# Kernel optimization log

Hardware: AMD Instinct MI355X
Metric: run time of the kernel (lower is better)

The kernel has to match this reference:

```python
import jax, jax.numpy as jnp
import numpy as np

TAU = 0.1  # args.aggregator_tau


def _l2_normalize(x, eps=1e-12):
    # F.normalize(x) : dim=1, p=2, eps clamp on the norm
    n = jnp.linalg.norm(x, axis=1, keepdims=True)
    return x / jnp.maximum(n, eps)


def setup_inputs() -> dict:
    key = jax.random.key(0)
    ks = jax.random.split(key, 9)
    N_LB, N_ULB, D, C = 4096, 6144, 128, 100
    return {
        "anchor_feat": jax.random.normal(ks[0], (N_ULB, D), dtype=jnp.float32),
        "positive_feat": jax.random.normal(ks[1], (N_ULB, D), dtype=jnp.float32),
        "lb_feat": jax.random.normal(ks[2], (N_LB, D), dtype=jnp.float32),
        "lb_one_hot": jax.random.uniform(ks[3], (N_LB, C), dtype=jnp.float32),
        "logits_x_lb": jax.random.normal(ks[4], (N_LB, C), dtype=jnp.float32),
        "logits_x_ulb_1": jax.random.normal(ks[5], (N_ULB, C), dtype=jnp.float32),
        "logits_x_ulb_2": jax.random.normal(ks[6], (N_ULB, C), dtype=jnp.float32),
        "labels_lb": jax.random.randint(ks[7], (N_LB,), 0, C, dtype=jnp.int64),
        "labels_ulb": jax.random.randint(ks[8], (N_ULB,), 0, C, dtype=jnp.int64),
    }


def reference(anchor_feat, positive_feat, lb_feat, lb_one_hot,
              logits_x_lb, logits_x_ulb_1, logits_x_ulb_2,
              labels_lb, labels_ulb):
    normed_lb = _l2_normalize(lb_feat)
    anchor_q = _l2_normalize(anchor_feat)
    positive_q = _l2_normalize(positive_feat)
    # [N, D] with N = N_lb + 2*N_ulb
    feats = jnp.concatenate([normed_lb, anchor_q, positive_q], axis=0)
    logits_before = jnp.concatenate([logits_x_lb, logits_x_ulb_1, logits_x_ulb_2], axis=0)  # [N, C]

    # topk(k=1) over classes
    pred_before = jnp.argmax(logits_before, axis=1)            # [N]
    max_before = jnp.max(logits_before, axis=1)                # [N]

    # non-parametric self-attention aggregation: softmax(FF^T/tau) @ logits
    sim = (feats @ feats.T) / TAU                              # [N, N] large intermediate
    attn = jax.nn.softmax(sim, axis=1)
    logits_after = attn @ logits_before                        # [N, C]

    pred_after = jnp.argmax(logits_after, axis=1)
    max_after = jnp.max(logits_after, axis=1)

    changed = pred_before != pred_after                        # [N] bool
    # Original applies Softmax(dim=1) to [M,1,1] slices of the k=1 top logits,
    # which is identically 1.0, so diff_agg is all zeros; replicate literally.
    diff = jnp.abs(jax.nn.softmax(max_before[:, None], axis=1)
                   - jax.nn.softmax(max_after[:, None], axis=1))[:, 0]  # [N], zeros

    # argmax/argmin restricted to changed indices (first changed idx under ties,
    # matching torch argmax over changed_pred_idx-ordered zeros)
    max_diff_idx = jnp.argmax(jnp.where(changed, diff, -jnp.inf))
    min_diff_idx = jnp.argmin(jnp.where(changed, diff, jnp.inf))

    pred_max_diff_bf = pred_before[max_diff_idx]
    pred_max_diff_af = pred_after[max_diff_idx]
    pred_min_diff_bf = pred_before[min_diff_idx]
    pred_min_diff_af = pred_after[min_diff_idx]

    num_lb = logits_x_lb.shape[0]
    out_lb = logits_after[:num_lb]
    out_ulb = logits_after[num_lb:]
    n_ulb = out_ulb.shape[0] // 2
    out_ulb_1, out_ulb_2 = out_ulb[:n_ulb], out_ulb[n_ulb:]

    return (anchor_feat, positive_feat, lb_feat, lb_one_hot,
            out_lb, out_ulb_1, out_ulb_2,
            max_diff_idx, min_diff_idx,
            pred_max_diff_bf, pred_max_diff_af,
            pred_min_diff_bf, pred_min_diff_af)
```

## Files before the change

### kernel.cpp

```cpp
#include <hip/hip_runtime.h>
#include <hip/hip_bf16.h>

typedef unsigned short u16;
typedef unsigned int u32;
typedef __attribute__((ext_vector_type(8))) short short8;
typedef __attribute__((ext_vector_type(4))) float f32x4;

#define N_LB   4096
#define N_ULB  6144
#define N_TOT  16384
#define D      128
#define C      100
#define CT     104

#define OFF_ANCHOR 0
#define OFF_POS    786432
#define OFF_LBF    1572864
#define OFF_OH     2097152
#define OFF_OUTLB  2506752
#define OFF_SCAL   4145152

__device__ __forceinline__ void split_bf16(float x, u16& hi, u16& lo) {
    __hip_bfloat16 h = __float2bfloat16(x);
    float r = x - __bfloat162float(h);
    __hip_bfloat16 l = __float2bfloat16(r);
    hi = __bfloat16_as_ushort(h);
    lo = __bfloat16_as_ushort(l);
}

__device__ __forceinline__ void gl_lds16(const char* g, char* l) {
    __builtin_amdgcn_global_load_lds(
        (const __attribute__((address_space(1))) u32*)g,
        (__attribute__((address_space(3))) u32*)l, 16, 0, 0);
}

__global__ void prep_feats(const float* __restrict__ anchor,
                           const float* __restrict__ positive,
                           const float* __restrict__ lbf,
                           u16* __restrict__ F2,
                           float* __restrict__ out)
{
    const int r = blockIdx.x;
    const int t = threadIdx.x;
    const float* src; int rr, ptbase;
    if (r < N_LB)              { src = lbf;      rr = r;                ptbase = OFF_LBF; }
    else if (r < N_LB + N_ULB) { src = anchor;   rr = r - N_LB;         ptbase = OFF_ANCHOR; }
    else                       { src = positive; rr = r - N_LB - N_ULB; ptbase = OFF_POS; }
    float2 x = *(const float2*)&src[rr * D + 2 * t];
    float ss = x.x * x.x + x.y * x.y;
    #pragma unroll
    for (int m = 32; m; m >>= 1) ss += __shfl_xor(ss, m);
    float inv = 1.0f / fmaxf(sqrtf(ss), 1e-12f);
    float y0 = x.x * inv, y1 = x.y * inv;
    u16 h0, l0, h1, l1;
    split_bf16(y0, h0, l0);
    split_bf16(y1, h1, l1);
    *(u32*)&F2[r * 256 + 2 * t]       = (u32)h0 | ((u32)h1 << 16);
    *(u32*)&F2[r * 256 + 128 + 2 * t] = (u32)l0 | ((u32)l1 << 16);
    *(float2*)&out[ptbase + rr * D + 2 * t] = x;
}

__global__ void prep_logits(const float* __restrict__ l_lb,
                            const float* __restrict__ l_u1,
                            const float* __restrict__ l_u2,
                            u16* __restrict__ LT,
                            int* __restrict__ predB)
{
    const int r = blockIdx.x;
    const int t = threadIdx.x;
    const float* src; int rr;
    if (r < N_LB)              { src = l_lb; rr = r; }
    else if (r < N_LB + N_ULB) { src = l_u1; rr = r - N_LB; }
    else                       { src = l_u2; rr = r - N_LB - N_ULB; }
    const int pc = (r & ~31) | (((r >> 2) & 3) << 3) | ((r & 3) << 1) | ((r >> 4) & 1);
    float v0 = src[rr * C + t];
    const int c1 = t + 64;
    float v1 = (c1 < C) ? src[rr * C + c1] : 0.0f;
    u16 h, l;
    split_bf16(v0, h, l);
    LT[(size_t)(0 * CT + t) * N_TOT + pc] = h;
    LT[(size_t)(1 * CT + t) * N_TOT + pc] = l;
    if (c1 < CT) {
        float v = (c1 < C) ? v1 : ((c1 == C) ? 1.0f : 0.0f);
        split_bf16(v, h, l);
        LT[(size_t)(0 * CT + c1) * N_TOT + pc] = h;
        LT[(size_t)(1 * CT + c1) * N_TOT + pc] = l;
    }
    float bv = v0; int bi = t;
    if (c1 < C && v1 > bv) { bv = v1; bi = c1; }
    #pragma unroll
    for (int m = 32; m; m >>= 1) {
        float ov = __shfl_xor(bv, m);
        int   oi = __shfl_xor(bi, m);
        if (ov > bv || (ov == bv && oi < bi)) { bv = ov; bi = oi; }
    }
    if (t == 0) predB[r] = bi;
}

__global__ void copy_oh(const float4* __restrict__ oh, float4* __restrict__ out)
{
    for (int i = blockIdx.x * blockDim.x + threadIdx.x; i < N_LB * C / 4;
         i += gridDim.x * blockDim.x)
        out[i] = oh[i];
}

#define SK_BYTES  (64 * 512)
#define SLT_BYTES (112 * 256)

__launch_bounds__(512)
__global__ void attn_mfma(const u16* __restrict__ F2, const u16* __restrict__ LT,
                          float* __restrict__ out)
{
    __shared__ __align__(16) char smem[2 * SK_BYTES + 2 * SLT_BYTES + 256];
    char* const sK0  = smem;
    char* const sK1  = smem + SK_BYTES;
    char* const sLT0 = smem + 2 * SK_BYTES;
    char* const sLT1 = smem + 2 * SK_BYTES + SLT_BYTES;
    float* const sInv = (float*)(smem + 2 * SK_BYTES + 2 * SLT_BYTES);

    const int tid  = threadIdx.x;
    const int lane = tid & 63;
    const int w    = tid >> 6;
    const int m    = w >> 1;
    const int nqh  = w & 1;
    const int g    = lane >> 4;
    const int lr   = lane & 15;
    const int r0   = blockIdx.x * 64;

    const char* F2b = (const char*)F2;
    const char* LTb = (const char*)LT;

    if (tid < 256) {
        char* dst = (tid >> 7) ? sLT1 : sLT0;
        int row = 104 + ((tid & 127) >> 4), gr = tid & 15;
        *(f32x4*)(dst + row * 256 + gr * 16) = f32x4{0, 0, 0, 0};
    }

    short8 qhi[4], qlo[4];
    {
        const char* base = F2b + (size_t)(r0 + m * 16 + lr) * 512;
        #pragma unroll
        for (int ks = 0; ks < 4; ++ks) {
            qhi[ks] = *(const short8*)(base + ks * 64 + g * 16);
            qlo[ks] = *(const short8*)(base + 256 + ks * 64 + g * 16);
        }
    }

    #pragma unroll
    for (int it = 0; it < 4; ++it) {
        int idx = tid + it * 512;
        int row = idx >> 5, b = (idx & 31) << 4;
        gl_lds16(F2b + (size_t)row * 512 + (b ^ ((row & 15) << 4)), sK0 + idx * 16);
    }
    #pragma unroll
    for (int it = 0; it < 4; ++it) {
        int idx = tid + it * 512;
        if (idx < 1664) {
            int row = idx >> 4, b = (idx & 15) << 4;
            int b2 = b ^ ((row & 7) << 4);
            int pl = b2 >> 7, kb = b2 & 127;
            gl_lds16(LTb + ((size_t)(pl * CT + row) * N_TOT) * 2 + kb, sLT0 + idx * 16);
        }
    }

    f32x4 o[7];
    #pragma unroll
    for (int ct = 0; ct < 7; ++ct) o[ct] = f32x4{0, 0, 0, 0};

    for (int ch = 0; ch < 256; ++ch) {
        const int cur = ch & 1;
        __syncthreads();

        if (ch + 1 < 256) {
            const int cn = (ch + 1) * 64;
            char* dK = cur ? sK0 : sK1;
            char* dL = cur ? sLT0 : sLT1;
            #pragma unroll
            for (int it = 0; it < 4; ++it) {
                int idx = tid + it * 512;
                int row = idx >> 5, b = (idx & 31) << 4;
                gl_lds16(F2b + (size_t)(cn + row) * 512 + (b ^ ((row & 15) << 4)),
                         dK + idx * 16);
            }
            #pragma unroll
            for (int it = 0; it < 4; ++it) {
                int idx = tid + it * 512;
                if (idx < 1664) {
                    int row = idx >> 4, b = (idx & 15) << 4;
                    int b2 = b ^ ((row & 7) << 4);
                    int pl = b2 >> 7, kb = b2 & 127;
                    gl_lds16(LTb + ((size_t)(pl * CT + row) * N_TOT + cn) * 2 + kb,
                             dL + idx * 16);
                }
            }
        }

        const char* K = cur ? sK1 : sK0;
        u16 h[2][4], l[2][4];
        #pragma unroll
        for (int t = 0; t < 2; ++t) {
            const int krow = nqh * 32 + t * 16 + lr;
            const int sw = (krow & 15) << 4;
            short8 khi[4], klo[4];
            #pragma unroll
            for (int ks = 0; ks < 4; ++ks) {
                int bo = ks * 64 + g * 16;
                khi[ks] = *(const short8*)(K + krow * 512 + (bo ^ sw));
                klo[ks] = *(const short8*)(K + krow * 512 + ((256 + bo) ^ sw));
            }
            f32x4 acc = {0, 0, 0, 0};
            #pragma unroll
            for (int ks = 0; ks < 4; ++ks)
                acc = __builtin_amdgcn_mfma_f32_16x16x32_bf16(khi[ks], qhi[ks], acc, 0, 0, 0);
            #pragma unroll
            for (int ks = 0; ks < 4; ++ks)
                acc = __builtin_amdgcn_mfma_f32_16x16x32_bf16(khi[ks], qlo[ks], acc, 0, 0, 0);
            #pragma unroll
            for (int ks = 0; ks < 4; ++ks)
                acc = __builtin_amdgcn_mfma_f32_16x16x32_bf16(klo[ks], qhi[ks], acc, 0, 0, 0);
            #pragma unroll
            for (int reg = 0; reg < 4; ++reg) {
                float p = __expf(10.0f * acc[reg] - 10.0f);
                split_bf16(p, h[t][reg], l[t][reg]);
            }
        }
        short8 Ahi = short8{(short)h[0][0], (short)h[1][0], (short)h[0][1], (short)h[1][1],
                            (short)h[0][2], (short)h[1][2], (short)h[0][3], (short)h[1][3]};
        short8 Alo = short8{(short)l[0][0], (short)l[1][0], (short)l[0][1], (short)l[1][1],
                            (short)l[0][2], (short)l[1][2], (short)l[0][3], (short)l[1][3]};

        const char* Lt = cur ? sLT1 : sLT0;
        #pragma unroll
        for (int ct = 0; ct < 7; ++ct) {
            int cls = ct * 16 + lr;
            int swc = (cls & 7) << 4;
            int boh = (nqh * 64 + g * 16) ^ swc;
            int bol = 128 + boh;
            short8 Bhi = *(const short8*)(Lt + cls * 256 + boh);
            short8 Blo = *(const short8*)(Lt + cls * 256 + bol);
            o[ct] = __builtin_amdgcn_mfma_f32_16x16x32_bf16(Ahi, Bhi, o[ct], 0, 0, 0);
            o[ct] = __builtin_amdgcn_mfma_f32_16x16x32_bf16(Ahi, Blo, o[ct], 0, 0, 0);
            o[ct] = __builtin_amdgcn_mfma_f32_16x16x32_bf16(Alo, Bhi, o[ct], 0, 0, 0);
        }
    }

    __syncthreads();
    float* red = (float*)smem;
    if (nqh == 1) {
        #pragma unroll
        for (int ct = 0; ct < 7; ++ct)
            #pragma unroll
            for (int reg = 0; reg < 4; ++reg)
                red[(m * 7 + ct) * 256 + reg * 64 + lane] = o[ct][reg];
    }
    __syncthreads();
    if (nqh == 0) {
        #pragma unroll
        for (int ct = 0; ct < 7; ++ct)
            #pragma unroll
            for (int reg = 0; reg < 4; ++reg)
                o[ct][reg] += red[(m * 7 + ct) * 256 + reg * 64 + lane];
        if (lr == 4) {
            #pragma unroll
            for (int reg = 0; reg < 4; ++reg)
                sInv[m * 16 + g * 4 + reg] = 1.0f / o[6][reg];
        }
    }
    __syncthreads();
    if (nqh == 0) {
        #pragma unroll
        for (int ct = 0; ct < 7; ++ct) {
            int cls = ct * 16 + lr;
            if (cls < C) {
                #pragma unroll
                for (int reg = 0; reg < 4; ++reg) {
                    int q = m * 16 + g * 4 + reg;
                    out[OFF_OUTLB + (size_t)(r0 + q) * C + cls] =
                        o[ct][reg] * sInv[q];
                }
            }
        }
    }
}

__global__ void argmax_after(const float* __restrict__ LA, int* __restrict__ predA)
{
    const int lane = threadIdx.x & 63;
    const int row  = blockIdx.x * 4 + (threadIdx.x >> 6);
    float bv = LA[row * C + lane]; int bi = lane;
    const int c1 = lane + 64;
    if (c1 < C) { float v1 = LA[row * C + c1]; if (v1 > bv) { bv = v1; bi = c1; } }
    #pragma unroll
    for (int m = 32; m; m >>= 1) {
        float ov = __shfl_xor(bv, m);
        int   oi = __shfl_xor(bi, m);
        if (ov > bv || (ov == bv && oi < bi)) { bv = ov; bi = oi; }
    }
    if (lane == 0) predA[row] = bi;
}

__global__ void finalize(const int* __restrict__ predA, const int* __restrict__ predB,
                         float* __restrict__ out)
{
    __shared__ int sm[256];
    const int t = threadIdx.x;
    int local = N_TOT;
    for (int r = t; r < N_TOT; r += 256)
        if (predA[r] != predB[r] && r < local) local = r;
    sm[t] = local;
    __syncthreads();
    for (int s = 128; s; s >>= 1) {
        if (t < s) sm[t] = min(sm[t], sm[t + s]);
        __syncthreads();
    }
    if (t == 0) {
        int first = (sm[0] == N_TOT) ? 0 : sm[0];
        out[OFF_SCAL + 0] = (float)first;
        out[OFF_SCAL + 1] = (float)first;
        out[OFF_SCAL + 2] = (float)predB[first];
        out[OFF_SCAL + 3] = (float)predA[first];
        out[OFF_SCAL + 4] = (float)predB[first];
        out[OFF_SCAL + 5] = (float)predA[first];
    }
}

extern "C" void kernel_launch(void* const* d_in, const int* in_sizes, int n_in,
                              void* d_out, int out_size, void* d_ws, size_t ws_size,
                              hipStream_t stream)
{
    const float* anchor   = (const float*)d_in[0];
    const float* positive = (const float*)d_in[1];
    const float* lbf      = (const float*)d_in[2];
    const float* oh       = (const float*)d_in[3];
    const float* l_lb     = (const float*)d_in[4];
    const float* l_u1     = (const float*)d_in[5];
    const float* l_u2     = (const float*)d_in[6];
    float* out = (float*)d_out;

    u16* F2 = (u16*)d_ws;
    u16* LT = F2 + (size_t)N_TOT * 256;
    int* predB = (int*)(LT + (size_t)2 * CT * N_TOT);
    int* predA = predB + N_TOT;

    prep_feats <<<N_TOT, 64, 0, stream>>>(anchor, positive, lbf, F2, out);
    prep_logits<<<N_TOT, 64, 0, stream>>>(l_lb, l_u1, l_u2, LT, predB);
    copy_oh    <<<200, 256, 0, stream>>>((const float4*)oh, (float4*)&out[OFF_OH]);
    attn_mfma  <<<256, 512, 0, stream>>>(F2, LT, out);
    argmax_after<<<N_TOT / 4, 256, 0, stream>>>(&out[OFF_OUTLB], predA);
    finalize   <<<1, 256, 0, stream>>>(predA, predB, out);
}
```

Measured before the change: 417.7 us.

## Give each wave two query subtiles in a 256-thread attention block

The attention kernel drops from 8 waves to 4 waves per block. Each wave now handles two 16-row query subtiles, so each K and LT fragment read from LDS feeds twice as many MFMAs and loads are amortised. The cost is more accumulator and query registers per wave, fewer waves to hide latency, and twice the cooperative copy work per thread for each chunk. The grid stays at 256 blocks, which on a chip with 256 CUs means one block per CU with lower occupancy.

Measured after the change: 448.0 us. 7.3% more time.

```diff
diff --git a/kernel.cpp b/kernel.cpp
--- a/kernel.cpp
+++ b/kernel.cpp
@@ -107,7 +107,7 @@
 #define SK_BYTES  (64 * 512)
 #define SLT_BYTES (112 * 256)
 
-__launch_bounds__(512)
+__launch_bounds__(256, 1)
 __global__ void attn_mfma(const u16* __restrict__ F2, const u16* __restrict__ LT,
                           float* __restrict__ out)
 {
@@ -121,7 +121,7 @@
     const int tid  = threadIdx.x;
     const int lane = tid & 63;
     const int w    = tid >> 6;
-    const int m    = w >> 1;
+    const int mh   = w >> 1;
     const int nqh  = w & 1;
     const int g    = lane >> 4;
     const int lr   = lane & 15;
@@ -130,31 +130,32 @@
     const char* F2b = (const char*)F2;
     const char* LTb = (const char*)LT;
 
-    if (tid < 256) {
+    {
         char* dst = (tid >> 7) ? sLT1 : sLT0;
         int row = 104 + ((tid & 127) >> 4), gr = tid & 15;
         *(f32x4*)(dst + row * 256 + gr * 16) = f32x4{0, 0, 0, 0};
     }
 
-    short8 qhi[4], qlo[4];
-    {
-        const char* base = F2b + (size_t)(r0 + m * 16 + lr) * 512;
+    short8 qhi[2][4], qlo[2][4];
+    #pragma unroll
+    for (int ms = 0; ms < 2; ++ms) {
+        const char* base = F2b + (size_t)(r0 + mh * 32 + ms * 16 + lr) * 512;
         #pragma unroll
         for (int ks = 0; ks < 4; ++ks) {
-            qhi[ks] = *(const short8*)(base + ks * 64 + g * 16);
-            qlo[ks] = *(const short8*)(base + 256 + ks * 64 + g * 16);
-        }
-    }
-
-    #pragma unroll
-    for (int it = 0; it < 4; ++it) {
-        int idx = tid + it * 512;
+            qhi[ms][ks] = *(const short8*)(base + ks * 64 + g * 16);
+            qlo[ms][ks] = *(const short8*)(base + 256 + ks * 64 + g * 16);
+        }
+    }
+
+    #pragma unroll
+    for (int it = 0; it < 8; ++it) {
+        int idx = tid + it * 256;
         int row = idx >> 5, b = (idx & 31) << 4;
         gl_lds16(F2b + (size_t)row * 512 + (b ^ ((row & 15) << 4)), sK0 + idx * 16);
     }
     #pragma unroll
-    for (int it = 0; it < 4; ++it) {
-        int idx = tid + it * 512;
+    for (int it = 0; it < 7; ++it) {
+        int idx = tid + it * 256;
         if (idx < 1664) {
             int row = idx >> 4, b = (idx & 15) << 4;
             int b2 = b ^ ((row & 7) << 4);
@@ -163,9 +164,11 @@
         }
     }
 
-    f32x4 o[7];
-    #pragma unroll
-    for (int ct = 0; ct < 7; ++ct) o[ct] = f32x4{0, 0, 0, 0};
+    f32x4 o[2][7];
+    #pragma unroll
+    for (int ms = 0; ms < 2; ++ms)
+        #pragma unroll
+        for (int ct = 0; ct < 7; ++ct) o[ms][ct] = f32x4{0, 0, 0, 0};
 
     for (int ch = 0; ch < 256; ++ch) {
         const int cur = ch & 1;
@@ -176,15 +179,15 @@
             char* dK = cur ? sK0 : sK1;
             char* dL = cur ? sLT0 : sLT1;
             #pragma unroll
-            for (int it = 0; it < 4; ++it) {
-                int idx = tid + it * 512;
+            for (int it = 0; it < 8; ++it) {
+                int idx = tid + it * 256;
                 int row = idx >> 5, b = (idx & 31) << 4;
                 gl_lds16(F2b + (size_t)(cn + row) * 512 + (b ^ ((row & 15) << 4)),
                          dK + idx * 16);
             }
             #pragma unroll
-            for (int it = 0; it < 4; ++it) {
-                int idx = tid + it * 512;
+            for (int it = 0; it < 7; ++it) {
+                int idx = tid + it * 256;
                 if (idx < 1664) {
                     int row = idx >> 4, b = (idx & 15) << 4;
                     int b2 = b ^ ((row & 7) << 4);
@@ -196,7 +199,7 @@
         }
 
         const char* K = cur ? sK1 : sK0;
-        u16 h[2][4], l[2][4];
+        u16 h[2][2][4], l[2][2][4];
         #pragma unroll
         for (int t = 0; t < 2; ++t) {
             const int krow = nqh * 32 + t * 16 + lr;
@@ -208,28 +211,39 @@
                 khi[ks] = *(const short8*)(K + krow * 512 + (bo ^ sw));
                 klo[ks] = *(const short8*)(K + krow * 512 + ((256 + bo) ^ sw));
             }
-            f32x4 acc = {0, 0, 0, 0};
-            #pragma unroll
-            for (int ks = 0; ks < 4; ++ks)
-                acc = __builtin_amdgcn_mfma_f32_16x16x32_bf16(khi[ks], qhi[ks], acc, 0, 0, 0);
-            #pragma unroll
-            for (int ks = 0; ks < 4; ++ks)
-                acc = __builtin_amdgcn_mfma_f32_16x16x32_bf16(khi[ks], qlo[ks], acc, 0, 0, 0);
-            #pragma unroll
-            for (int ks = 0; ks < 4; ++ks)
-                acc = __builtin_amdgcn_mfma_f32_16x16x32_bf16(klo[ks], qhi[ks], acc, 0, 0, 0);
-            #pragma unroll
-            for (int reg = 0; reg < 4; ++reg) {
-                float p = __expf(10.0f * acc[reg] - 10.0f);
-                split_bf16(p, h[t][reg], l[t][reg]);
-            }
-        }
-        short8 Ahi = short8{(short)h[0][0], (short)h[1][0], (short)h[0][1], (short)h[1][1],
-                            (short)h[0][2], (short)h[1][2], (short)h[0][3], (short)h[1][3]};
-        short8 Alo = short8{(short)l[0][0], (short)l[1][0], (short)l[0][1], (short)l[1][1],
-                            (short)l[0][2], (short)l[1][2], (short)l[0][3], (short)l[1][3]};
+            #pragma unroll
+            for (int ms = 0; ms < 2; ++ms) {
+                f32x4 acc = {0, 0, 0, 0};
+                #pragma unroll
+                for (int ks = 0; ks < 4; ++ks)
+                    acc = __builtin_amdgcn_mfma_f32_16x16x32_bf16(khi[ks], qhi[ms][ks], acc, 0, 0, 0);
+                #pragma unroll
+                for (int ks = 0; ks < 4; ++ks)
+                    acc = __builtin_amdgcn_mfma_f32_16x16x32_bf16(khi[ks], qlo[ms][ks], acc, 0, 0, 0);
+                #pragma unroll
+                for (int ks = 0; ks < 4; ++ks)
+                    acc = __builtin_amdgcn_mfma_f32_16x16x32_bf16(klo[ks], qhi[ms][ks], acc, 0, 0, 0);
+                #pragma unroll
+                for (int reg = 0; reg < 4; ++reg) {
+                    float p = __expf(10.0f * acc[reg] - 10.0f);
+                    split_bf16(p, h[ms][t][reg], l[ms][t][reg]);
+                }
+            }
+        }
 
         const char* Lt = cur ? sLT1 : sLT0;
+        short8 Ahi[2], Alo[2];
+        #pragma unroll
+        for (int ms = 0; ms < 2; ++ms) {
+            Ahi[ms] = short8{(short)h[ms][0][0], (short)h[ms][1][0],
+                             (short)h[ms][0][1], (short)h[ms][1][1],
+                             (short)h[ms][0][2], (short)h[ms][1][2],
+                             (short)h[ms][0][3], (short)h[ms][1][3]};
+            Alo[ms] = short8{(short)l[ms][0][0], (short)l[ms][1][0],
+                             (short)l[ms][0][1], (short)l[ms][1][1],
+                             (short)l[ms][0][2], (short)l[ms][1][2],
+                             (short)l[ms][0][3], (short)l[ms][1][3]};
+        }
         #pragma unroll
         for (int ct = 0; ct < 7; ++ct) {
             int cls = ct * 16 + lr;
@@ -238,9 +252,12 @@
             int bol = 128 + boh;
             short8 Bhi = *(const short8*)(Lt + cls * 256 + boh);
             short8 Blo = *(const short8*)(Lt + cls * 256 + bol);
-            o[ct] = __builtin_amdgcn_mfma_f32_16x16x32_bf16(Ahi, Bhi, o[ct], 0, 0, 0);
-            o[ct] = __builtin_amdgcn_mfma_f32_16x16x32_bf16(Ahi, Blo, o[ct], 0, 0, 0);
-            o[ct] = __builtin_amdgcn_mfma_f32_16x16x32_bf16(Alo, Bhi, o[ct], 0, 0, 0);
+            #pragma unroll
+            for (int ms = 0; ms < 2; ++ms) {
+                o[ms][ct] = __builtin_amdgcn_mfma_f32_16x16x32_bf16(Ahi[ms], Bhi, o[ms][ct], 0, 0, 0);
+                o[ms][ct] = __builtin_amdgcn_mfma_f32_16x16x32_bf16(Ahi[ms], Blo, o[ms][ct], 0, 0, 0);
+                o[ms][ct] = __builtin_amdgcn_mfma_f32_16x16x32_bf16(Alo[ms], Bhi, o[ms][ct], 0, 0, 0);
+            }
         }
     }
 
@@ -248,35 +265,44 @@
     float* red = (float*)smem;
     if (nqh == 1) {
         #pragma unroll
-        for (int ct = 0; ct < 7; ++ct)
-            #pragma unroll
-            for (int reg = 0; reg < 4; ++reg)
-                red[(m * 7 + ct) * 256 + reg * 64 + lane] = o[ct][reg];
+        for (int ms = 0; ms < 2; ++ms)
+            #pragma unroll
+            for (int ct = 0; ct < 7; ++ct)
+                #pragma unroll
+                for (int reg = 0; reg < 4; ++reg)
+                    red[((mh * 2 + ms) * 7 + ct) * 256 + reg * 64 + lane] = o[ms][ct][reg];
     }
     __syncthreads();
     if (nqh == 0) {
         #pragma unroll
-        for (int ct = 0; ct < 7; ++ct)
-            #pragma unroll
-            for (int reg = 0; reg < 4; ++reg)
-                o[ct][reg] += red[(m * 7 + ct) * 256 + reg * 64 + lane];
+        for (int ms = 0; ms < 2; ++ms)
+            #pragma unroll
+            for (int ct = 0; ct < 7; ++ct)
+                #pragma unroll
+                for (int reg = 0; reg < 4; ++reg)
+                    o[ms][ct][reg] += red[((mh * 2 + ms) * 7 + ct) * 256 + reg * 64 + lane];
         if (lr == 4) {
             #pragma unroll
-            for (int reg = 0; reg < 4; ++reg)
-                sInv[m * 16 + g * 4 + reg] = 1.0f / o[6][reg];
+            for (int ms = 0; ms < 2; ++ms)
+                #pragma unroll
+                for (int reg = 0; reg < 4; ++reg)
+                    sInv[mh * 32 + ms * 16 + g * 4 + reg] = 1.0f / o[ms][6][reg];
         }
     }
     __syncthreads();
     if (nqh == 0) {
         #pragma unroll
-        for (int ct = 0; ct < 7; ++ct) {
-            int cls = ct * 16 + lr;
-            if (cls < C) {
-                #pragma unroll
-                for (int reg = 0; reg < 4; ++reg) {
-                    int q = m * 16 + g * 4 + reg;
-                    out[OFF_OUTLB + (size_t)(r0 + q) * C + cls] =
-                        o[ct][reg] * sInv[q];
+        for (int ms = 0; ms < 2; ++ms) {
+            #pragma unroll
+            for (int ct = 0; ct < 7; ++ct) {
+                int cls = ct * 16 + lr;
+                if (cls < C) {
+                    #pragma unroll
+                    for (int reg = 0; reg < 4; ++reg) {
+                        int q = mh * 32 + ms * 16 + g * 4 + reg;
+                        out[OFF_OUTLB + (size_t)(r0 + q) * C + cls] =
+                            o[ms][ct][reg] * sInv[q];
+                    }
                 }
             }
         }
@@ -345,7 +371,7 @@
     prep_feats <<<N_TOT, 64, 0, stream>>>(anchor, positive, lbf, F2, out);
     prep_logits<<<N_TOT, 64, 0, stream>>>(l_lb, l_u1, l_u2, LT, predB);
     copy_oh    <<<200, 256, 0, stream>>>((const float4*)oh, (float4*)&out[OFF_OH]);
-    attn_mfma  <<<256, 512, 0, stream>>>(F2, LT, out);
+    attn_mfma  <<<256, 256, 0, stream>>>(F2, LT, out);
     argmax_after<<<N_TOT / 4, 256, 0, stream>>>(&out[OFF_OUTLB], predA);
     finalize   <<<1, 256, 0, stream>>>(predA, predB, out);
 }
```
